# Kernel tuning notes

Measured on AMD Instinct MI355X. Metric: run time of the kernel, lower is better.

Reference implementation:

```python
import jax, jax.numpy as jnp
import numpy as np

B, T, PHYS = 256, 64, 3        # batch of initial conditions, time steps, physical dim
LAT, NN, NHID = 8, 128, 3      # latent dim, hidden width, num hidden layers
WIN, PRED = 32, 64             # Hankel window, num_pred_steps


def _mlp(x, w_in, b_in, w_h, b_h, w_out, b_out):
    # Dense stack: relu hidden layers, linear output (ae_output_activation='linear')
    h = jax.nn.relu(x @ w_in + b_in)
    for i in range(w_h.shape[0]):
        h = jax.nn.relu(h @ w_h[i] + b_h[i])
    return h @ w_out + b_out


def _hankel_dmd(y):
    # y: [B, L, T] latent trajectories (already transposed as in call())
    Bsz, L, Tn = y.shape
    R = Tn - (WIN - 1)                                   # num_rows_hankel
    # Vectorized Hankel build (replaces nested TensorArray loops):
    idx = jnp.arange(R)[:, None] + jnp.arange(WIN)[None, :]
    H = y[:, :, idx].reshape(Bsz, L * R, WIN)
    Ym, Yp = H[:, :, :-1], H[:, :, 1:]
    # Exact DMD operator A = Yp V Sig^-1 U^H (full M x M, as in the TF code)
    U, sig, Vh = jnp.linalg.svd(Ym, full_matrices=False)
    V = jnp.swapaxes(Vh, -1, -2)
    A = Yp @ (V / sig[:, None, :]) @ jnp.swapaxes(U, -1, -2)     # [B, M, M]
    A = jax.lax.stop_gradient(A)   # no-op in fwd; eig has no JAX grad rule
    evals, evecs = jnp.linalg.eig(A)                             # complex64: [B,M], [B,M,M]
    Phi = jnp.linalg.solve(evecs, Ym.astype(evecs.dtype))
    y0 = Phi[:, :, 0]                                            # [B, M]
    evecs_s = evecs[:, ::R, :]                                   # stride = R -> [B, L, M]
    # Vectorized replacement of the sequential recon loop: evals^k for k=0..P-1
    powers = evals[:, None, :] ** jnp.arange(PRED)[None, :, None]  # [B, P, M]
    modes = powers * y0[:, None, :]                                # [B, P, M]
    recon = jnp.real(jnp.einsum('blm,bpm->bpl', evecs_s, modes))   # [B, P, L]
    return recon


def setup_inputs() -> dict:
    ks = jax.random.split(jax.random.key(0), 8)

    def w(k, fi, fo):
        return jax.random.normal(k, (fi, fo), jnp.float32) / np.sqrt(fi)

    def wh(k, f):
        return jax.random.normal(k, (NHID, f, f), jnp.float32) / np.sqrt(f)

    return {
        'x': jax.random.normal(ks[0], (B, T, PHYS), jnp.float32),
        'enc_w_in': w(ks[1], PHYS, NN), 'enc_b_in': jnp.zeros((NN,), jnp.float32),
        'enc_w_h': wh(ks[2], NN), 'enc_b_h': jnp.zeros((NHID, NN), jnp.float32),
        'enc_w_out': w(ks[3], NN, LAT), 'enc_b_out': jnp.zeros((LAT,), jnp.float32),
        'dec_w_in': w(ks[4], LAT, NN), 'dec_b_in': jnp.zeros((NN,), jnp.float32),
        'dec_w_h': wh(ks[5], NN), 'dec_b_h': jnp.zeros((NHID, NN), jnp.float32),
        'dec_w_out': w(ks[6], NN, PHYS), 'dec_b_out': jnp.zeros((PHYS,), jnp.float32),
    }


def reference(x, enc_w_in, enc_b_in, enc_w_h, enc_b_h, enc_w_out, enc_b_out,
              dec_w_in, dec_b_in, dec_w_h, dec_b_h, dec_w_out, dec_b_out):
    y = _mlp(x, enc_w_in, enc_b_in, enc_w_h, enc_b_h, enc_w_out, enc_b_out)        # [B, T, LAT]
    x_ae = _mlp(y, dec_w_in, dec_b_in, dec_w_h, dec_b_h, dec_w_out, dec_b_out)     # [B, T, PHYS]
    y_adv = _hankel_dmd(jnp.swapaxes(y, 1, 2))                                     # [B, PRED, LAT]
    x_adv = _mlp(y_adv, dec_w_in, dec_b_in, dec_w_h, dec_b_h, dec_w_out, dec_b_out)  # [B, PRED, PHYS]
    return (y, x_ae, x_adv, y_adv)
```

## Files before the change

### kernel.cpp

```cpp
#include <hip/hip_runtime.h>
#include <math.h>

namespace {
constexpr int kB = 256;
constexpr int kT = 64;
constexpr int kPhys = 3;
constexpr int kLat = 8;
constexpr int kNN = 128;
constexpr int kWin = 32;
constexpr int kPred = 64;
constexpr int kHPad = 132;
constexpr int kDecRows = 96;
constexpr int kFragElems = 6 * 4 * 64 * 8;
}

typedef short bf16x8 __attribute__((ext_vector_type(8)));
typedef float f32x4 __attribute__((ext_vector_type(4)));

__device__ __forceinline__ double rdlane_f64(double x, int l) {
  const long long v = __double_as_longlong(x);
  const int lo = __builtin_amdgcn_readlane((int)(unsigned int)(v & 0xffffffffll), l);
  const int hi = __builtin_amdgcn_readlane((int)(v >> 32), l);
  const long long r = (((long long)hi) << 32) | (unsigned long long)(unsigned int)lo;
  return __longlong_as_double(r);
}

__device__ __forceinline__ unsigned rneb(float f) {
  const unsigned u = __float_as_uint(f);
  return (u + 0x7fffu + ((u >> 16) & 1u)) >> 16;
}
__device__ __forceinline__ void split3(float a, short& s1, short& s2, short& s3) {
  const unsigned b1 = rneb(a);
  const float f1 = __uint_as_float(b1 << 16);
  const float r1 = a - f1;
  const unsigned b2 = rneb(r1);
  const float f2 = __uint_as_float(b2 << 16);
  const float r2 = r1 - f2;
  const unsigned b3 = rneb(r2);
  s1 = (short)b1; s2 = (short)b2; s3 = (short)b3;
}

template<int MT, bool TO_FRAG>
__device__ __forceinline__ void mfma_layer(
    const float* __restrict__ W, const float* __restrict__ bias,
    const short* __restrict__ A1, const short* __restrict__ A2,
    const short* __restrict__ A3,
    short* __restrict__ D1, short* __restrict__ D2, short* __restrict__ D3,
    float* __restrict__ hbout, int tid)
{
  const int wid = tid >> 6, l = tid & 63;
  const int colg = 16 * wid + (l & 15);
  const int krow = 8 * (l >> 4);
  bf16x8 B1[4], B2[4], B3[4];
#pragma unroll
  for (int q = 0; q < 4; ++q) {
#pragma unroll
    for (int e = 0; e < 8; ++e) {
      const float w = W[(32 * q + krow + e) * kNN + colg];
      short s1, s2, s3; split3(w, s1, s2, s3);
      B1[q][e] = s1; B2[q][e] = s2; B3[q][e] = s3;
    }
  }
  const float bj = bias[colg];
  const int qt = colg >> 5, sub = (colg >> 3) & 3, et = colg & 7;
  const int rbase = (l >> 4) * 4;
#pragma unroll
  for (int mp = 0; mp < MT; mp += 2) {
    f32x4 acc0 = {bj, bj, bj, bj}, acc1 = {bj, bj, bj, bj};
#pragma unroll
    for (int q = 0; q < 4; ++q) {
      const int o0 = ((mp * 4 + q) * 64 + l) * 8;
      const int o1 = (((mp + 1) * 4 + q) * 64 + l) * 8;
      const bf16x8 a01 = *(const bf16x8*)&A1[o0];
      const bf16x8 a02 = *(const bf16x8*)&A2[o0];
      const bf16x8 a03 = *(const bf16x8*)&A3[o0];
      const bf16x8 a11 = *(const bf16x8*)&A1[o1];
      const bf16x8 a12 = *(const bf16x8*)&A2[o1];
      const bf16x8 a13 = *(const bf16x8*)&A3[o1];
      acc0 = __builtin_amdgcn_mfma_f32_16x16x32_bf16(a01, B1[q], acc0, 0, 0, 0);
      acc1 = __builtin_amdgcn_mfma_f32_16x16x32_bf16(a11, B1[q], acc1, 0, 0, 0);
      acc0 = __builtin_amdgcn_mfma_f32_16x16x32_bf16(a01, B2[q], acc0, 0, 0, 0);
      acc1 = __builtin_amdgcn_mfma_f32_16x16x32_bf16(a11, B2[q], acc1, 0, 0, 0);
      acc0 = __builtin_amdgcn_mfma_f32_16x16x32_bf16(a02, B1[q], acc0, 0, 0, 0);
      acc1 = __builtin_amdgcn_mfma_f32_16x16x32_bf16(a12, B1[q], acc1, 0, 0, 0);
      acc0 = __builtin_amdgcn_mfma_f32_16x16x32_bf16(a01, B3[q], acc0, 0, 0, 0);
      acc1 = __builtin_amdgcn_mfma_f32_16x16x32_bf16(a11, B3[q], acc1, 0, 0, 0);
      acc0 = __builtin_amdgcn_mfma_f32_16x16x32_bf16(a02, B2[q], acc0, 0, 0, 0);
      acc1 = __builtin_amdgcn_mfma_f32_16x16x32_bf16(a12, B2[q], acc1, 0, 0, 0);
      acc0 = __builtin_amdgcn_mfma_f32_16x16x32_bf16(a03, B1[q], acc0, 0, 0, 0);
      acc1 = __builtin_amdgcn_mfma_f32_16x16x32_bf16(a13, B1[q], acc1, 0, 0, 0);
    }
#pragma unroll
    for (int half = 0; half < 2; ++half) {
      const int m = mp + half;
#pragma unroll
      for (int r = 0; r < 4; ++r) {
        const float v = fmaxf(half ? acc1[r] : acc0[r], 0.f);
        if constexpr (TO_FRAG) {
          short s1, s2, s3; split3(v, s1, s2, s3);
          const int off = ((m * 4 + qt) * 64 + (rbase + r + 16 * sub)) * 8 + et;
          D1[off] = s1; D2[off] = s2; D3[off] = s3;
        } else {
          hbout[(m * 16 + rbase + r) * kHPad + colg] = v;
        }
      }
    }
  }
}

__global__ __launch_bounds__(512) void fused_kernel(
    const float* __restrict__ x,
    const float* __restrict__ ewin, const float* __restrict__ ebin,
    const float* __restrict__ ewh,  const float* __restrict__ ebh,
    const float* __restrict__ ewout,const float* __restrict__ ebout,
    const float* __restrict__ dwin, const float* __restrict__ dbin,
    const float* __restrict__ dwh,  const float* __restrict__ dbh,
    const float* __restrict__ dwout,const float* __restrict__ dbout,
    float* __restrict__ y_g, float* __restrict__ xae_g,
    float* __restrict__ xadv_g, float* __restrict__ yadv_g)
{
  __shared__ __align__(16) char regA[kFragElems * 3 * 2];
  __shared__ __align__(16) char regB[kFragElems * 3 * 2];
  __shared__ float ybuf[kT][kLat + 1];
  __shared__ float yadv2[kWin][kLat + 1];
  __shared__ float inb[kT][4];

  short* sA1 = (short*)regA;
  short* sA2 = sA1 + kFragElems;
  short* sA3 = sA2 + kFragElems;
  short* sB1 = (short*)regB;
  short* sB2 = sB1 + kFragElems;
  short* sB3 = sB2 + kFragElems;
  float* hb  = (float*)regB;

  const int tid = threadIdx.x;
  const int b = blockIdx.x;

  const float* __restrict__ xg = x + (size_t)b * kT * kPhys;
  for (int i = tid; i < kT * kPhys; i += 512) inb[i / 3][i % 3] = xg[i];
  __syncthreads();

  {
    const int j = tid & 127, rh = tid >> 7;
    const float w0 = ewin[j], w1 = ewin[kNN + j], w2 = ewin[2 * kNN + j];
    const float bj = ebin[j];
    const int qt = j >> 5, sub = (j >> 3) & 3, et = j & 7;
#pragma unroll
    for (int c = 0; c < 16; ++c) {
      const int r = 4 * c + rh;
      const float a = fmaxf(bj + inb[r][0] * w0 + inb[r][1] * w1 + inb[r][2] * w2, 0.f);
      short s1, s2, s3; split3(a, s1, s2, s3);
      const int off = (((r >> 4) * 4 + qt) * 64 + ((r & 15) + 16 * sub)) * 8 + et;
      sA1[off] = s1; sA2[off] = s2; sA3[off] = s3;
    }
  }
  __syncthreads();
  mfma_layer<4, true >(ewh,                 ebh,           sA1, sA2, sA3, sB1, sB2, sB3, hb, tid);
  __syncthreads();
  mfma_layer<4, true >(ewh + 1 * kNN * kNN, ebh + 1 * kNN, sB1, sB2, sB3, sA1, sA2, sA3, hb, tid);
  __syncthreads();
  mfma_layer<4, false>(ewh + 2 * kNN * kNN, ebh + 2 * kNN, sA1, sA2, sA3, sB1, sB2, sB3, hb, tid);
  __syncthreads();

  {
    const int r = tid >> 3, o = tid & 7;
    float a = ebout[o];
    for (int k4 = 0; k4 < kNN; k4 += 4) {
      const float4 hv = *(const float4*)&hb[r * kHPad + k4];
      a += hv.x * ewout[(k4 + 0) * kLat + o] + hv.y * ewout[(k4 + 1) * kLat + o]
         + hv.z * ewout[(k4 + 2) * kLat + o] + hv.w * ewout[(k4 + 3) * kLat + o];
    }
    ybuf[r][o] = a;
    y_g[(size_t)b * kT * kLat + tid] = a;
  }
  __syncthreads();

  {
    double (*yd)[kT + 1]  = (double(*)[kT + 1])(regA);
    double (*P)[67]       = (double(*)[67])(regA + 4160);
    double (*Corr)[33]    = (double(*)[33])(regA + 21312);
    double (*KTm)[33]     = (double(*)[33])(regA + 29760);
    double (*Dv)[33]      = (double(*)[33])(regA + 37944);

    yd[tid & 7][tid >> 3] = (double)ybuf[tid >> 3][tid & 7];
    __syncthreads();

    for (int idx = tid; idx < 32 * 64; idx += 512) {
      const int d = idx >> 6, t = idx & 63;
      if (t + d < kT) {
        double s = 0.0;
#pragma unroll
        for (int l = 0; l < kLat; ++l) s += yd[l][t] * yd[l][t + d];
        P[d][t] = s;
      }
    }
    __syncthreads();

    for (int idx = tid; idx < 32 * 32; idx += 512) {
      const int a = idx >> 5, c = idx & 31;
      const int d = (c >= a) ? (c - a) : (a - c);
      const int base = (c >= a) ? a : c;
      double s0 = 0.0, s1 = 0.0;
#pragma unroll
      for (int r = 0; r < 32; r += 2) { s0 += P[d][base + r]; s1 += P[d][base + r + 1]; }
      Corr[a][c] = s0 + s1 + P[d][base + 32];
    }
    __syncthreads();

    if (tid < 64) {
      const int lane = tid;
      const int colidx = (lane <= 30) ? lane : (lane <= 61 ? lane - 30 : 1);
      double m[31];
#pragma unroll
      for (int i = 0; i < 31; ++i) m[i] = Corr[i][colidx];
#pragma unroll
      for (int k = 0; k < 31; ++k) {
        const double piv = rdlane_f64(m[k], k);
        const double pinv = 1.0 / piv;
        m[k] *= pinv;
#pragma unroll
        for (int i = 0; i < 31; ++i) {
          if (i == k) continue;
          const double bci = rdlane_f64(m[i], k);
          m[i] = fma(-bci, m[k], m[i]);
        }
      }
      if (lane >= 31 && lane < 62) {
        const int c = lane - 31;
#pragma unroll
        for (int i = 0; i < 31; ++i) KTm[i][c] = m[i];
      }
      const int ri = (lane < 31) ? lane : 0;
      double Kr[31];
#pragma unroll
      for (int j = 0; j < 31; ++j) Kr[j] = KTm[ri][j];

      double dv = Kr[30];
      if (lane < 31) Dv[0][lane] = dv;
      for (int k = 0; k < 31; ++k) {
        double a0 = 0.0, a1 = 0.0, a2 = 0.0, a3 = 0.0;
#pragma unroll
        for (int j = 0; j < 31; ++j) {
          const double dj = rdlane_f64(dv, j);
          if ((j & 3) == 0) a0 = fma(Kr[j], dj, a0);
          else if ((j & 3) == 1) a1 = fma(Kr[j], dj, a1);
          else if ((j & 3) == 2) a2 = fma(Kr[j], dj, a2);
          else a3 = fma(Kr[j], dj, a3);
        }
        dv = (a0 + a1) + (a2 + a3);
        if (lane < 31) Dv[k + 1][lane] = dv;
      }
    }
    __syncthreads();

    float* __restrict__ ob = yadv_g + (size_t)b * kPred * kLat;
    if (tid < 256) {
      ob[tid] = ybuf[tid >> 3][tid & 7];
    } else {
      const int q = tid - 256;
      const int k = q >> 3, l = q & 7;
      double a0 = 0.0, a1 = 0.0, a2 = 0.0, a3 = 0.0;
#pragma unroll
      for (int j = 0; j < 31; ++j) {
        if ((j & 3) == 0) a0 = fma(yd[l][j + 1], Dv[k][j], a0);
        else if ((j & 3) == 1) a1 = fma(yd[l][j + 1], Dv[k][j], a1);
        else if ((j & 3) == 2) a2 = fma(yd[l][j + 1], Dv[k][j], a2);
        else a3 = fma(yd[l][j + 1], Dv[k][j], a3);
      }
      const float v = (float)((a0 + a1) + (a2 + a3));
      ob[256 + q] = v;
      yadv2[k][l] = v;
    }
    __syncthreads();
  }

  {
    const int j = tid & 127, rh = tid >> 7;
    float wr[kLat];
#pragma unroll
    for (int k = 0; k < kLat; ++k) wr[k] = dwin[k * kNN + j];
    const float bj = dbin[j];
    const int qt = j >> 5, sub = (j >> 3) & 3, et = j & 7;
#pragma unroll
    for (int c = 0; c < 24; ++c) {
      const int r = 4 * c + rh;
      const float* __restrict__ src = (r < kT) ? &ybuf[r][0] : &yadv2[r - kT][0];
      float a = bj;
#pragma unroll
      for (int k = 0; k < kLat; ++k) a += src[k] * wr[k];
      a = fmaxf(a, 0.f);
      short s1, s2, s3; split3(a, s1, s2, s3);
      const int off = (((r >> 4) * 4 + qt) * 64 + ((r & 15) + 16 * sub)) * 8 + et;
      sA1[off] = s1; sA2[off] = s2; sA3[off] = s3;
    }
  }
  __syncthreads();
  mfma_layer<6, true >(dwh,                 dbh,           sA1, sA2, sA3, sB1, sB2, sB3, hb, tid);
  __syncthreads();
  mfma_layer<6, true >(dwh + 1 * kNN * kNN, dbh + 1 * kNN, sB1, sB2, sB3, sA1, sA2, sA3, hb, tid);
  __syncthreads();
  mfma_layer<6, false>(dwh + 2 * kNN * kNN, dbh + 2 * kNN, sA1, sA2, sA3, sB1, sB2, sB3, hb, tid);
  __syncthreads();

  for (int idx = tid; idx < kDecRows * kPhys; idx += 512) {
    const int r = idx / 3, o = idx - r * 3;
    float a = dbout[o];
    for (int k4 = 0; k4 < kNN; k4 += 4) {
      const float4 hv = *(const float4*)&hb[r * kHPad + k4];
      a += hv.x * dwout[(k4 + 0) * kPhys + o] + hv.y * dwout[(k4 + 1) * kPhys + o]
         + hv.z * dwout[(k4 + 2) * kPhys + o] + hv.w * dwout[(k4 + 3) * kPhys + o];
    }
    if (r < kT) {
      xae_g[(size_t)b * kT * kPhys + idx] = a;
      if (r < kWin) xadv_g[(size_t)b * kT * kPhys + idx] = a;
    } else {
      const int rr = r - kT + kWin;
      xadv_g[(size_t)b * kT * kPhys + rr * kPhys + o] = a;
    }
  }
}

extern "C" void kernel_launch(void* const* d_in, const int* in_sizes, int n_in,
                              void* d_out, int out_size, void* d_ws, size_t ws_size,
                              hipStream_t stream)
{
  const float* x         = (const float*)d_in[0];
  const float* enc_w_in  = (const float*)d_in[1];
  const float* enc_b_in  = (const float*)d_in[2];
  const float* enc_w_h   = (const float*)d_in[3];
  const float* enc_b_h   = (const float*)d_in[4];
  const float* enc_w_out = (const float*)d_in[5];
  const float* enc_b_out = (const float*)d_in[6];
  const float* dec_w_in  = (const float*)d_in[7];
  const float* dec_b_in  = (const float*)d_in[8];
  const float* dec_w_h   = (const float*)d_in[9];
  const float* dec_b_h   = (const float*)d_in[10];
  const float* dec_w_out = (const float*)d_in[11];
  const float* dec_b_out = (const float*)d_in[12];

  float* out   = (float*)d_out;
  float* y     = out;
  float* x_ae  = out + (size_t)kB * kT * kLat;
  float* x_adv = x_ae + (size_t)kB * kT * kPhys;
  float* y_adv = x_adv + (size_t)kB * kT * kPhys;

  fused_kernel<<<kB, 512, 0, stream>>>(
      x, enc_w_in, enc_b_in, enc_w_h, enc_b_h, enc_w_out, enc_b_out,
      dec_w_in, dec_b_in, dec_w_h, dec_b_h, dec_w_out, dec_b_out,
      y, x_ae, x_adv, y_adv);
}
```

Baseline: 61.62 us.

## Double threads per block, separate fp32 staging and fragment packing, 2-split decoder

Launches 1024 threads per block so each wave handles fewer row tiles of the MLP MFMA layers. Activations are stored in fp32 and converted to bf16 split fragments in a separate vectorized packing pass. The decoder layers switch from a 3-way to a 2-way bf16 split, halving their MFMA count. This adds an extra pass and barrier per layer and lowers decoder precision.

```diff
diff --git a/kernel.cpp b/kernel.cpp
--- a/kernel.cpp
+++ b/kernel.cpp
@@ -9,9 +9,9 @@
 constexpr int kNN = 128;
 constexpr int kWin = 32;
 constexpr int kPred = 64;
-constexpr int kHPad = 132;
+constexpr int kHRow = 132;
 constexpr int kDecRows = 96;
-constexpr int kFragElems = 6 * 4 * 64 * 8;
+constexpr int kThreads = 1024;
 }
 
 typedef short bf16x8 __attribute__((ext_vector_type(8)));
@@ -35,80 +35,100 @@
   const float r1 = a - f1;
   const unsigned b2 = rneb(r1);
   const float f2 = __uint_as_float(b2 << 16);
-  const float r2 = r1 - f2;
-  const unsigned b3 = rneb(r2);
-  s1 = (short)b1; s2 = (short)b2; s3 = (short)b3;
-}
-
-template<int MT, bool TO_FRAG>
+  s1 = (short)b1; s2 = (short)b2; s3 = (short)rneb(r1 - f2);
+}
+__device__ __forceinline__ void split2(float a, short& s1, short& s2) {
+  const unsigned b1 = rneb(a);
+  const float f1 = __uint_as_float(b1 << 16);
+  s1 = (short)b1; s2 = (short)rneb(a - f1);
+}
+
+template<int MT, int SPLITS>
+__device__ __forceinline__ void pack_frag(const float* __restrict__ hb,
+                                          short* __restrict__ frag, int tid)
+{
+  constexpr int PLANE = MT * 4 * 64 * 8;
+  for (int idx = tid; idx < MT * 256; idx += kThreads) {
+    const int m = idx >> 8, q = (idx >> 6) & 3, l = idx & 63;
+    const int row = 16 * m + (l & 15), col = 32 * q + 8 * (l >> 4);
+    const float4 f0 = *(const float4*)&hb[row * kHRow + col];
+    const float4 f1 = *(const float4*)&hb[row * kHRow + col + 4];
+    const float f[8] = {f0.x, f0.y, f0.z, f0.w, f1.x, f1.y, f1.z, f1.w};
+    bf16x8 p1, p2, p3;
+#pragma unroll
+    for (int e = 0; e < 8; ++e) {
+      if constexpr (SPLITS == 3) {
+        short s1, s2, s3; split3(f[e], s1, s2, s3);
+        p1[e] = s1; p2[e] = s2; p3[e] = s3;
+      } else {
+        short s1, s2; split2(f[e], s1, s2);
+        p1[e] = s1; p2[e] = s2;
+      }
+    }
+    const int o = ((m * 4 + q) * 64 + l) * 8;
+    *(bf16x8*)&frag[o] = p1;
+    *(bf16x8*)&frag[PLANE + o] = p2;
+    if constexpr (SPLITS == 3) *(bf16x8*)&frag[2 * PLANE + o] = p3;
+  }
+}
+
+template<int MPW, int SPLITS>
 __device__ __forceinline__ void mfma_layer(
     const float* __restrict__ W, const float* __restrict__ bias,
-    const short* __restrict__ A1, const short* __restrict__ A2,
-    const short* __restrict__ A3,
-    short* __restrict__ D1, short* __restrict__ D2, short* __restrict__ D3,
-    float* __restrict__ hbout, int tid)
+    const short* __restrict__ frag, float* __restrict__ hb, int tid)
 {
-  const int wid = tid >> 6, l = tid & 63;
-  const int colg = 16 * wid + (l & 15);
+  constexpr int MT = 2 * MPW;
+  constexpr int PLANE = MT * 4 * 64 * 8;
+  const int w = tid >> 6, l = tid & 63;
+  const int n = w & 7, m0 = (w >> 3) * MPW;
+  const int colg = 16 * n + (l & 15);
   const int krow = 8 * (l >> 4);
   bf16x8 B1[4], B2[4], B3[4];
 #pragma unroll
   for (int q = 0; q < 4; ++q) {
 #pragma unroll
     for (int e = 0; e < 8; ++e) {
-      const float w = W[(32 * q + krow + e) * kNN + colg];
-      short s1, s2, s3; split3(w, s1, s2, s3);
-      B1[q][e] = s1; B2[q][e] = s2; B3[q][e] = s3;
+      const float wv = W[(32 * q + krow + e) * kNN + colg];
+      if constexpr (SPLITS == 3) {
+        short s1, s2, s3; split3(wv, s1, s2, s3);
+        B1[q][e] = s1; B2[q][e] = s2; B3[q][e] = s3;
+      } else {
+        short s1, s2; split2(wv, s1, s2);
+        B1[q][e] = s1; B2[q][e] = s2;
+      }
     }
   }
   const float bj = bias[colg];
-  const int qt = colg >> 5, sub = (colg >> 3) & 3, et = colg & 7;
+  f32x4 acc[MPW];
+#pragma unroll
+  for (int mi = 0; mi < MPW; ++mi) acc[mi] = {bj, bj, bj, bj};
+#pragma unroll
+  for (int q = 0; q < 4; ++q) {
+#pragma unroll
+    for (int mi = 0; mi < MPW; ++mi) {
+      const int o = (((m0 + mi) * 4 + q) * 64 + l) * 8;
+      const bf16x8 a1 = *(const bf16x8*)&frag[o];
+      const bf16x8 a2 = *(const bf16x8*)&frag[PLANE + o];
+      acc[mi] = __builtin_amdgcn_mfma_f32_16x16x32_bf16(a1, B1[q], acc[mi], 0, 0, 0);
+      acc[mi] = __builtin_amdgcn_mfma_f32_16x16x32_bf16(a1, B2[q], acc[mi], 0, 0, 0);
+      acc[mi] = __builtin_amdgcn_mfma_f32_16x16x32_bf16(a2, B1[q], acc[mi], 0, 0, 0);
+      if constexpr (SPLITS == 3) {
+        const bf16x8 a3 = *(const bf16x8*)&frag[2 * PLANE + o];
+        acc[mi] = __builtin_amdgcn_mfma_f32_16x16x32_bf16(a1, B3[q], acc[mi], 0, 0, 0);
+        acc[mi] = __builtin_amdgcn_mfma_f32_16x16x32_bf16(a2, B2[q], acc[mi], 0, 0, 0);
+        acc[mi] = __builtin_amdgcn_mfma_f32_16x16x32_bf16(a3, B1[q], acc[mi], 0, 0, 0);
+      }
+    }
+  }
   const int rbase = (l >> 4) * 4;
 #pragma unroll
-  for (int mp = 0; mp < MT; mp += 2) {
-    f32x4 acc0 = {bj, bj, bj, bj}, acc1 = {bj, bj, bj, bj};
-#pragma unroll
-    for (int q = 0; q < 4; ++q) {
-      const int o0 = ((mp * 4 + q) * 64 + l) * 8;
-      const int o1 = (((mp + 1) * 4 + q) * 64 + l) * 8;
-      const bf16x8 a01 = *(const bf16x8*)&A1[o0];
-      const bf16x8 a02 = *(const bf16x8*)&A2[o0];
-      const bf16x8 a03 = *(const bf16x8*)&A3[o0];
-      const bf16x8 a11 = *(const bf16x8*)&A1[o1];
-      const bf16x8 a12 = *(const bf16x8*)&A2[o1];
-      const bf16x8 a13 = *(const bf16x8*)&A3[o1];
-      acc0 = __builtin_amdgcn_mfma_f32_16x16x32_bf16(a01, B1[q], acc0, 0, 0, 0);
-      acc1 = __builtin_amdgcn_mfma_f32_16x16x32_bf16(a11, B1[q], acc1, 0, 0, 0);
-      acc0 = __builtin_amdgcn_mfma_f32_16x16x32_bf16(a01, B2[q], acc0, 0, 0, 0);
-      acc1 = __builtin_amdgcn_mfma_f32_16x16x32_bf16(a11, B2[q], acc1, 0, 0, 0);
-      acc0 = __builtin_amdgcn_mfma_f32_16x16x32_bf16(a02, B1[q], acc0, 0, 0, 0);
-      acc1 = __builtin_amdgcn_mfma_f32_16x16x32_bf16(a12, B1[q], acc1, 0, 0, 0);
-      acc0 = __builtin_amdgcn_mfma_f32_16x16x32_bf16(a01, B3[q], acc0, 0, 0, 0);
-      acc1 = __builtin_amdgcn_mfma_f32_16x16x32_bf16(a11, B3[q], acc1, 0, 0, 0);
-      acc0 = __builtin_amdgcn_mfma_f32_16x16x32_bf16(a02, B2[q], acc0, 0, 0, 0);
-      acc1 = __builtin_amdgcn_mfma_f32_16x16x32_bf16(a12, B2[q], acc1, 0, 0, 0);
-      acc0 = __builtin_amdgcn_mfma_f32_16x16x32_bf16(a03, B1[q], acc0, 0, 0, 0);
-      acc1 = __builtin_amdgcn_mfma_f32_16x16x32_bf16(a13, B1[q], acc1, 0, 0, 0);
-    }
-#pragma unroll
-    for (int half = 0; half < 2; ++half) {
-      const int m = mp + half;
-#pragma unroll
-      for (int r = 0; r < 4; ++r) {
-        const float v = fmaxf(half ? acc1[r] : acc0[r], 0.f);
-        if constexpr (TO_FRAG) {
-          short s1, s2, s3; split3(v, s1, s2, s3);
-          const int off = ((m * 4 + qt) * 64 + (rbase + r + 16 * sub)) * 8 + et;
-          D1[off] = s1; D2[off] = s2; D3[off] = s3;
-        } else {
-          hbout[(m * 16 + rbase + r) * kHPad + colg] = v;
-        }
-      }
-    }
-  }
-}
-
-__global__ __launch_bounds__(512) void fused_kernel(
+  for (int mi = 0; mi < MPW; ++mi)
+#pragma unroll
+    for (int r = 0; r < 4; ++r)
+      hb[(16 * (m0 + mi) + rbase + r) * kHRow + colg] = fmaxf(acc[mi][r], 0.f);
+}
+
+__global__ __launch_bounds__(kThreads, 4) void fused_kernel(
     const float* __restrict__ x,
     const float* __restrict__ ewin, const float* __restrict__ ebin,
     const float* __restrict__ ewh,  const float* __restrict__ ebh,
@@ -119,54 +139,45 @@
     float* __restrict__ y_g, float* __restrict__ xae_g,
     float* __restrict__ xadv_g, float* __restrict__ yadv_g)
 {
-  __shared__ __align__(16) char regA[kFragElems * 3 * 2];
-  __shared__ __align__(16) char regB[kFragElems * 3 * 2];
+  __shared__ float hb[kDecRows * kHRow];
+  __shared__ __align__(16) char fragbuf[49152];
   __shared__ float ybuf[kT][kLat + 1];
   __shared__ float yadv2[kWin][kLat + 1];
   __shared__ float inb[kT][4];
 
-  short* sA1 = (short*)regA;
-  short* sA2 = sA1 + kFragElems;
-  short* sA3 = sA2 + kFragElems;
-  short* sB1 = (short*)regB;
-  short* sB2 = sB1 + kFragElems;
-  short* sB3 = sB2 + kFragElems;
-  float* hb  = (float*)regB;
-
+  short* frag = (short*)fragbuf;
   const int tid = threadIdx.x;
   const int b = blockIdx.x;
 
   const float* __restrict__ xg = x + (size_t)b * kT * kPhys;
-  for (int i = tid; i < kT * kPhys; i += 512) inb[i / 3][i % 3] = xg[i];
+  for (int i = tid; i < kT * kPhys; i += kThreads) inb[i / 3][i % 3] = xg[i];
   __syncthreads();
 
   {
-    const int j = tid & 127, rh = tid >> 7;
+    const int j = tid & 127, rg = tid >> 7;
     const float w0 = ewin[j], w1 = ewin[kNN + j], w2 = ewin[2 * kNN + j];
     const float bj = ebin[j];
-    const int qt = j >> 5, sub = (j >> 3) & 3, et = j & 7;
-#pragma unroll
-    for (int c = 0; c < 16; ++c) {
-      const int r = 4 * c + rh;
-      const float a = fmaxf(bj + inb[r][0] * w0 + inb[r][1] * w1 + inb[r][2] * w2, 0.f);
-      short s1, s2, s3; split3(a, s1, s2, s3);
-      const int off = (((r >> 4) * 4 + qt) * 64 + ((r & 15) + 16 * sub)) * 8 + et;
-      sA1[off] = s1; sA2[off] = s2; sA3[off] = s3;
+#pragma unroll
+    for (int rr = 0; rr < 8; ++rr) {
+      const int r = rg * 8 + rr;
+      hb[r * kHRow + j] = fmaxf(bj + inb[r][0] * w0 + inb[r][1] * w1 + inb[r][2] * w2, 0.f);
     }
   }
   __syncthreads();
-  mfma_layer<4, true >(ewh,                 ebh,           sA1, sA2, sA3, sB1, sB2, sB3, hb, tid);
-  __syncthreads();
-  mfma_layer<4, true >(ewh + 1 * kNN * kNN, ebh + 1 * kNN, sB1, sB2, sB3, sA1, sA2, sA3, hb, tid);
-  __syncthreads();
-  mfma_layer<4, false>(ewh + 2 * kNN * kNN, ebh + 2 * kNN, sA1, sA2, sA3, sB1, sB2, sB3, hb, tid);
-  __syncthreads();
-
-  {
+
+#pragma unroll
+  for (int L = 0; L < 3; ++L) {
+    pack_frag<4, 3>(hb, frag, tid);
+    __syncthreads();
+    mfma_layer<2, 3>(ewh + (size_t)L * kNN * kNN, ebh + L * kNN, frag, hb, tid);
+    __syncthreads();
+  }
+
+  if (tid < 512) {
     const int r = tid >> 3, o = tid & 7;
     float a = ebout[o];
     for (int k4 = 0; k4 < kNN; k4 += 4) {
-      const float4 hv = *(const float4*)&hb[r * kHPad + k4];
+      const float4 hv = *(const float4*)&hb[r * kHRow + k4];
       a += hv.x * ewout[(k4 + 0) * kLat + o] + hv.y * ewout[(k4 + 1) * kLat + o]
          + hv.z * ewout[(k4 + 2) * kLat + o] + hv.w * ewout[(k4 + 3) * kLat + o];
     }
@@ -176,34 +187,35 @@
   __syncthreads();
 
   {
-    double (*yd)[kT + 1]  = (double(*)[kT + 1])(regA);
-    double (*P)[67]       = (double(*)[67])(regA + 4160);
-    double (*Corr)[33]    = (double(*)[33])(regA + 21312);
-    double (*KTm)[33]     = (double(*)[33])(regA + 29760);
-    double (*Dv)[33]      = (double(*)[33])(regA + 37944);
-
-    yd[tid & 7][tid >> 3] = (double)ybuf[tid >> 3][tid & 7];
-    __syncthreads();
-
-    for (int idx = tid; idx < 32 * 64; idx += 512) {
+    double* dmd = (double*)fragbuf;
+    double* yd   = dmd;
+    double* P    = dmd + 520;
+    double* Corr = dmd + 2664;
+    double* KTm  = dmd + 3720;
+    double* Dv   = dmd + 4743;
+
+    if (tid < 512) yd[(tid & 7) * 65 + (tid >> 3)] = (double)ybuf[tid >> 3][tid & 7];
+    __syncthreads();
+
+    for (int idx = tid; idx < 32 * 64; idx += kThreads) {
       const int d = idx >> 6, t = idx & 63;
       if (t + d < kT) {
         double s = 0.0;
 #pragma unroll
-        for (int l = 0; l < kLat; ++l) s += yd[l][t] * yd[l][t + d];
-        P[d][t] = s;
-      }
-    }
-    __syncthreads();
-
-    for (int idx = tid; idx < 32 * 32; idx += 512) {
-      const int a = idx >> 5, c = idx & 31;
+        for (int l = 0; l < kLat; ++l) s += yd[l * 65 + t] * yd[l * 65 + t + d];
+        P[d * 67 + t] = s;
+      }
+    }
+    __syncthreads();
+
+    if (tid < 1024) {
+      const int a = tid >> 5, c = tid & 31;
       const int d = (c >= a) ? (c - a) : (a - c);
       const int base = (c >= a) ? a : c;
       double s0 = 0.0, s1 = 0.0;
 #pragma unroll
-      for (int r = 0; r < 32; r += 2) { s0 += P[d][base + r]; s1 += P[d][base + r + 1]; }
-      Corr[a][c] = s0 + s1 + P[d][base + 32];
+      for (int r = 0; r < 32; r += 2) { s0 += P[d * 67 + base + r]; s1 += P[d * 67 + base + r + 1]; }
+      Corr[a * 33 + c] = s0 + s1 + P[d * 67 + base + 32];
     }
     __syncthreads();
 
@@ -212,7 +224,7 @@
       const int colidx = (lane <= 30) ? lane : (lane <= 61 ? lane - 30 : 1);
       double m[31];
 #pragma unroll
-      for (int i = 0; i < 31; ++i) m[i] = Corr[i][colidx];
+      for (int i = 0; i < 31; ++i) m[i] = Corr[i * 33 + colidx];
 #pragma unroll
       for (int k = 0; k < 31; ++k) {
         const double piv = rdlane_f64(m[k], k);
@@ -228,15 +240,15 @@
       if (lane >= 31 && lane < 62) {
         const int c = lane - 31;
 #pragma unroll
-        for (int i = 0; i < 31; ++i) KTm[i][c] = m[i];
+        for (int i = 0; i < 31; ++i) KTm[i * 33 + c] = m[i];
       }
       const int ri = (lane < 31) ? lane : 0;
       double Kr[31];
 #pragma unroll
-      for (int j = 0; j < 31; ++j) Kr[j] = KTm[ri][j];
+      for (int j = 0; j < 31; ++j) Kr[j] = KTm[ri * 33 + j];
 
       double dv = Kr[30];
-      if (lane < 31) Dv[0][lane] = dv;
+      if (lane < 31) Dv[0 * 33 + lane] = dv;
       for (int k = 0; k < 31; ++k) {
         double a0 = 0.0, a1 = 0.0, a2 = 0.0, a3 = 0.0;
 #pragma unroll
@@ -248,7 +260,7 @@
           else a3 = fma(Kr[j], dj, a3);
         }
         dv = (a0 + a1) + (a2 + a3);
-        if (lane < 31) Dv[k + 1][lane] = dv;
+        if (lane < 31) Dv[(k + 1) * 33 + lane] = dv;
       }
     }
     __syncthreads();
@@ -256,16 +268,17 @@
     float* __restrict__ ob = yadv_g + (size_t)b * kPred * kLat;
     if (tid < 256) {
       ob[tid] = ybuf[tid >> 3][tid & 7];
-    } else {
+    } else if (tid < 512) {
       const int q = tid - 256;
       const int k = q >> 3, l = q & 7;
       double a0 = 0.0, a1 = 0.0, a2 = 0.0, a3 = 0.0;
 #pragma unroll
       for (int j = 0; j < 31; ++j) {
-        if ((j & 3) == 0) a0 = fma(yd[l][j + 1], Dv[k][j], a0);
-        else if ((j & 3) == 1) a1 = fma(yd[l][j + 1], Dv[k][j], a1);
-        else if ((j & 3) == 2) a2 = fma(yd[l][j + 1], Dv[k][j], a2);
-        else a3 = fma(yd[l][j + 1], Dv[k][j], a3);
+        const double t = yd[l * 65 + j + 1] ;
+        if ((j & 3) == 0) a0 = fma(t, Dv[k * 33 + j], a0);
+        else if ((j & 3) == 1) a1 = fma(t, Dv[k * 33 + j], a1);
+        else if ((j & 3) == 2) a2 = fma(t, Dv[k * 33 + j], a2);
+        else a3 = fma(t, Dv[k * 33 + j], a3);
       }
       const float v = (float)((a0 + a1) + (a2 + a3));
       ob[256 + q] = v;
@@ -275,38 +288,36 @@
   }
 
   {
-    const int j = tid & 127, rh = tid >> 7;
+    const int j = tid & 127, rg = tid >> 7;
     float wr[kLat];
 #pragma unroll
     for (int k = 0; k < kLat; ++k) wr[k] = dwin[k * kNN + j];
     const float bj = dbin[j];
-    const int qt = j >> 5, sub = (j >> 3) & 3, et = j & 7;
-#pragma unroll
-    for (int c = 0; c < 24; ++c) {
-      const int r = 4 * c + rh;
+#pragma unroll
+    for (int rr = 0; rr < 12; ++rr) {
+      const int r = rg * 12 + rr;
       const float* __restrict__ src = (r < kT) ? &ybuf[r][0] : &yadv2[r - kT][0];
       float a = bj;
 #pragma unroll
       for (int k = 0; k < kLat; ++k) a += src[k] * wr[k];
-      a = fmaxf(a, 0.f);
-      short s1, s2, s3; split3(a, s1, s2, s3);
-      const int off = (((r >> 4) * 4 + qt) * 64 + ((r & 15) + 16 * sub)) * 8 + et;
-      sA1[off] = s1; sA2[off] = s2; sA3[off] = s3;
+      hb[r * kHRow + j] = fmaxf(a, 0.f);
     }
   }
   __syncthreads();
-  mfma_layer<6, true >(dwh,                 dbh,           sA1, sA2, sA3, sB1, sB2, sB3, hb, tid);
-  __syncthreads();
-  mfma_layer<6, true >(dwh + 1 * kNN * kNN, dbh + 1 * kNN, sB1, sB2, sB3, sA1, sA2, sA3, hb, tid);
-  __syncthreads();
-  mfma_layer<6, false>(dwh + 2 * kNN * kNN, dbh + 2 * kNN, sA1, sA2, sA3, sB1, sB2, sB3, hb, tid);
-  __syncthreads();
-
-  for (int idx = tid; idx < kDecRows * kPhys; idx += 512) {
+
+#pragma unroll
+  for (int L = 0; L < 3; ++L) {
+    pack_frag<6, 2>(hb, frag, tid);
+    __syncthreads();
+    mfma_layer<3, 2>(dwh + (size_t)L * kNN * kNN, dbh + L * kNN, frag, hb, tid);
+    __syncthreads();
+  }
+
+  for (int idx = tid; idx < kDecRows * kPhys; idx += kThreads) {
     const int r = idx / 3, o = idx - r * 3;
     float a = dbout[o];
     for (int k4 = 0; k4 < kNN; k4 += 4) {
-      const float4 hv = *(const float4*)&hb[r * kHPad + k4];
+      const float4 hv = *(const float4*)&hb[r * kHRow + k4];
       a += hv.x * dwout[(k4 + 0) * kPhys + o] + hv.y * dwout[(k4 + 1) * kPhys + o]
          + hv.z * dwout[(k4 + 2) * kPhys + o] + hv.w * dwout[(k4 + 3) * kPhys + o];
     }
@@ -344,7 +355,7 @@
   float* x_adv = x_ae + (size_t)kB * kT * kPhys;
   float* y_adv = x_adv + (size_t)kB * kT * kPhys;
 
-  fused_kernel<<<kB, 512, 0, stream>>>(
+  fused_kernel<<<kB, kThreads, 0, stream>>>(
       x, enc_w_in, enc_b_in, enc_w_h, enc_b_h, enc_w_out, enc_b_out,
       dec_w_in, dec_b_in, dec_w_h, dec_b_h, dec_w_out, dec_b_out,
       y, x_ae, x_adv, y_adv);
```

Result: no change. 60.43 us (-1.9%).
